# Kernel tuning notes

Hardware: AMD Instinct MI355X
Metric: run time of the kernel (lower is better)

Reference implementation:

```python
import jax, jax.numpy as jnp
import numpy as np

ROUTINGS = 3
EPS = 1e-7  # K.epsilon()


def squash(s, axis=-1):
    # v = (||s||^2 / (1 + ||s||^2)) * s / ||s||
    s_sq = jnp.sum(jnp.square(s), axis=axis, keepdims=True)
    scale = s_sq / (1.0 + s_sq) / jnp.sqrt(s_sq + EPS)
    return scale * s


def setup_inputs() -> dict:
    key = jax.random.key(0)
    k1, k2 = jax.random.split(key)
    B, num_in_caps, in_caps_dim = 32, 2048, 16
    num_caps, caps_dim = 64, 32
    input_tensor = jax.random.normal(k1, (B, num_in_caps, in_caps_dim), dtype=jnp.float32)
    # he_normal init: std = sqrt(2 / fan_in), fan_in = in_caps_dim (last axis contracted)
    fan_in = num_in_caps * caps_dim * in_caps_dim  # keras computes fan_in from receptive field; use simple he scale
    W = jax.random.normal(k2, (num_caps, num_in_caps, caps_dim, in_caps_dim), dtype=jnp.float32) * np.float32(np.sqrt(2.0 / in_caps_dim))
    return {"input_tensor": input_tensor, "W": W}


def reference(input_tensor, W):
    B = input_tensor.shape[0]
    num_caps, num_in_caps = W.shape[0], W.shape[1]
    # inputs_hat[b,j,i,c] = sum_d W[j,i,c,d] * x[b,i,d]  (fused einsum replacing map_fn+batch_dot)
    inputs_hat = jnp.einsum('bid,jicd->bjic', input_tensor, W)
    b = jnp.zeros((B, num_caps, num_in_caps), dtype=inputs_hat.dtype)
    # NOTE: source never updates b inside the loop, so every iteration is identical.
    activations = None
    for _ in range(ROUTINGS):
        c = jax.nn.softmax(b, axis=1)  # over num_caps axis, as tf.nn.softmax(b, dim=1)
        s = jnp.einsum('bji,bjic->bjc', c, inputs_hat)  # batch_dot(c, inputs_hat, [2,2])
        activations = squash(s)
    return activations
```

## Files before the change

kernel.cpp:

```cpp
#include <hip/hip_runtime.h>

typedef __attribute__((ext_vector_type(8)))  short bf16x8;
typedef __attribute__((ext_vector_type(16))) float f32x16;
typedef __attribute__((ext_vector_type(4)))  int   i32x4;

__device__ __forceinline__ unsigned cvt2(float lo, float hi) {
    unsigned r;
    asm volatile("v_cvt_pk_bf16_f32 %0, %1, %2" : "=v"(r) : "v"(lo), "v"(hi));
    return r;
}
__device__ __forceinline__ bf16x8 pack8(float4 a, float4 b) {
    union { i32x4 i; bf16x8 h; } c;
    c.i.x = cvt2(a.x, a.y);
    c.i.y = cvt2(a.z, a.w);
    c.i.z = cvt2(b.x, b.y);
    c.i.w = cvt2(b.z, b.w);
    return c.h;
}

__global__ void caps_init(float* __restrict__ ws) {
    ws[blockIdx.x * 256 + threadIdx.x] = 0.0f;
}

template<int MODE>
__global__ __launch_bounds__(256, 4)
void caps_mfma(const float* __restrict__ x, const float* __restrict__ W,
               float* __restrict__ ws)
{
    const int tid  = threadIdx.x;
    const int w    = tid >> 6;
    const int lane = tid & 63;
    const int m    = lane & 31;
    const int h    = lane >> 5;

    const int j     = blockIdx.x >> 4;
    const int ic    = blockIdx.x & 15;
    const int ibase = ic * 128;

    const char* Wb = (const char*)W + (((size_t)(j * 2048 + ibase + w)) << 11)
                   + (m << 6) + (h << 5);
    const char* Xb = (const char*)x + ((size_t)m << 17) + ((ibase + w) << 6) + (h << 5);

    f32x16 acc = {};

    float4 wv[4][2], xv[4][2];
#pragma unroll
    for (int s = 0; s < 4; ++s) {
        wv[s][0] = *(const float4*)(Wb + s * 8192);
        wv[s][1] = *(const float4*)(Wb + s * 8192 + 16);
        xv[s][0] = *(const float4*)(Xb + s * 256);
        xv[s][1] = *(const float4*)(Xb + s * 256 + 16);
    }

#pragma unroll 1
    for (int t = 0; t < 28; t += 4) {
#pragma unroll
        for (int s = 0; s < 4; ++s) {
            bf16x8 afrag = pack8(xv[s][0], xv[s][1]);
            bf16x8 bfrag = pack8(wv[s][0], wv[s][1]);
            wv[s][0] = *(const float4*)(Wb + (s + 4) * 8192);
            wv[s][1] = *(const float4*)(Wb + (s + 4) * 8192 + 16);
            xv[s][0] = *(const float4*)(Xb + (s + 4) * 256);
            xv[s][1] = *(const float4*)(Xb + (s + 4) * 256 + 16);
            acc = __builtin_amdgcn_mfma_f32_32x32x16_bf16(afrag, bfrag, acc, 0, 0, 0);
        }
        Wb += 4 * 8192; Xb += 4 * 256;
    }
#pragma unroll
    for (int s = 0; s < 4; ++s)
        acc = __builtin_amdgcn_mfma_f32_32x32x16_bf16(
                  pack8(xv[s][0], xv[s][1]), pack8(wv[s][0], wv[s][1]), acc, 0, 0, 0);

    __shared__ float red[4096];
#pragma unroll
    for (int r = 0; r < 16; ++r)
        red[w * 1024 + r * 64 + lane] = acc[r];
    __syncthreads();

#pragma unroll
    for (int e = 0; e < 4; ++e) {
        int idx = e * 256 + tid;
        int b = idx >> 5, c = idx & 31;
        int l = (((b >> 2) & 1) << 5) + c;
        int r = (b & 3) | (((b >> 3) & 3) << 2);
        float s = red[r * 64 + l] + red[1024 + r * 64 + l]
                + red[2048 + r * 64 + l] + red[3072 + r * 64 + l];
        if (MODE == 0)
            ws[(ic * 32 + b) * 2048 + j * 32 + c] = s;
        else
            atomicAdd(&ws[b * 2048 + j * 32 + c], s);
    }
}

template<int NIC>
__global__ void caps_finalize(const float* __restrict__ ws, float* __restrict__ out) {
    int o = blockIdx.x * 256 + threadIdx.x;
    int b = o >> 11;
    int rest = o & 2047;
    float v = 0.0f;
#pragma unroll
    for (int k = 0; k < NIC; ++k) v += ws[(k * 32 + b) * 2048 + rest];
    v *= (1.0f / 64.0f);
    float sq = v * v;
    sq += __shfl_xor(sq, 1, 64);
    sq += __shfl_xor(sq, 2, 64);
    sq += __shfl_xor(sq, 4, 64);
    sq += __shfl_xor(sq, 8, 64);
    sq += __shfl_xor(sq, 16, 64);
    float scale = sq / (1.0f + sq) / sqrtf(sq + 1e-7f);
    out[o] = scale * v;
}

__global__ void caps_finalize_a(const float* __restrict__ ws, float* __restrict__ out) {
    int o = blockIdx.x * 256 + threadIdx.x;
    float v = ws[o] * (1.0f / 64.0f);
    float sq = v * v;
    sq += __shfl_xor(sq, 1, 64);
    sq += __shfl_xor(sq, 2, 64);
    sq += __shfl_xor(sq, 4, 64);
    sq += __shfl_xor(sq, 8, 64);
    sq += __shfl_xor(sq, 16, 64);
    float scale = sq / (1.0f + sq) / sqrtf(sq + 1e-7f);
    out[o] = scale * v;
}

extern "C" void kernel_launch(void* const* d_in, const int* in_sizes, int n_in,
                              void* d_out, int out_size, void* d_ws, size_t ws_size,
                              hipStream_t stream) {
    (void)in_sizes; (void)n_in; (void)out_size;
    const float* x = (const float*)d_in[0];
    const float* W = (const float*)d_in[1];
    float* out = (float*)d_out;
    float* ws  = (float*)d_ws;

    if (ws_size >= (size_t)16 * 65536 * sizeof(float)) {
        hipLaunchKernelGGL((caps_mfma<0>),     dim3(1024), dim3(256), 0, stream, x, W, ws);
        hipLaunchKernelGGL((caps_finalize<16>),dim3(256),  dim3(256), 0, stream, ws, out);
    } else {
        float* acc_buf = (ws_size >= (size_t)65536 * sizeof(float)) ? ws : out;
        hipLaunchKernelGGL(caps_init,          dim3(256),  dim3(256), 0, stream, acc_buf);
        hipLaunchKernelGGL((caps_mfma<1>),     dim3(1024), dim3(256), 0, stream, x, W, acc_buf);
        hipLaunchKernelGGL(caps_finalize_a,    dim3(256),  dim3(256), 0, stream, acc_buf, out);
    }
}
```

Before: 60.70 us.

## Pre-convert x to bf16 fragment layout and halve input-capsule chunk size

Adds a pre-pass kernel that converts x to bf16 and stores it in the exact per-lane MFMA A-fragment order. The main kernel then loads x with one contiguous 16-byte load per step instead of strided fp32 gathers plus conversion. The i-chunk size also drops from 128 to 64, doubling the grid to 2048 blocks for more parallelism. The cost is an extra launch, a larger workspace slab, and twice the partial sums for finalize to reduce.

```diff
diff --git a/kernel.cpp b/kernel.cpp
--- a/kernel.cpp
+++ b/kernel.cpp
@@ -18,58 +18,87 @@
     return c.h;
 }
 
+__global__ void caps_xconv(const float* __restrict__ x, uint4* __restrict__ xf) {
+    int g = blockIdx.x * 256 + threadIdx.x;
+    int i = g >> 6, l = g & 63;
+    int b = l & 31, h = l >> 5;
+    const float4* p = (const float4*)(x + (b * 2048 + i) * 16 + h * 8);
+    float4 a = p[0], q = p[1];
+    uint4 o;
+    o.x = cvt2(a.x, a.y); o.y = cvt2(a.z, a.w);
+    o.z = cvt2(q.x, q.y); o.w = cvt2(q.z, q.w);
+    xf[g] = o;
+}
+
 __global__ void caps_init(float* __restrict__ ws) {
     ws[blockIdx.x * 256 + threadIdx.x] = 0.0f;
 }
 
-template<int MODE>
+template<int MODE, int GATHER, int ICHUNK>
 __global__ __launch_bounds__(256, 4)
 void caps_mfma(const float* __restrict__ x, const float* __restrict__ W,
-               float* __restrict__ ws)
+               float* __restrict__ ws, const char* __restrict__ xf)
 {
+    constexpr int NIC = 2048 / ICHUNK;
+    constexpr int NT  = ICHUNK / 4;
+
     const int tid  = threadIdx.x;
     const int w    = tid >> 6;
     const int lane = tid & 63;
     const int m    = lane & 31;
     const int h    = lane >> 5;
 
-    const int j     = blockIdx.x >> 4;
-    const int ic    = blockIdx.x & 15;
-    const int ibase = ic * 128;
+    const int j     = blockIdx.x / NIC;
+    const int ic    = blockIdx.x % NIC;
+    const int ibase = ic * ICHUNK;
 
     const char* Wb = (const char*)W + (((size_t)(j * 2048 + ibase + w)) << 11)
                    + (m << 6) + (h << 5);
     const char* Xb = (const char*)x + ((size_t)m << 17) + ((ibase + w) << 6) + (h << 5);
+    const char* Xf = xf + ((ibase + w) << 10) + (lane << 4);
 
     f32x16 acc = {};
 
-    float4 wv[4][2], xv[4][2];
+    float4 wv[4][2];
+    bf16x8 xa[4];
+    float4 xg[4][2];
+
 #pragma unroll
     for (int s = 0; s < 4; ++s) {
         wv[s][0] = *(const float4*)(Wb + s * 8192);
         wv[s][1] = *(const float4*)(Wb + s * 8192 + 16);
-        xv[s][0] = *(const float4*)(Xb + s * 256);
-        xv[s][1] = *(const float4*)(Xb + s * 256 + 16);
+        if (GATHER) {
+            xg[s][0] = *(const float4*)(Xb + s * 256);
+            xg[s][1] = *(const float4*)(Xb + s * 256 + 16);
+        } else {
+            xa[s] = *(const bf16x8*)(Xf + s * 4096);
+        }
     }
 
 #pragma unroll 1
-    for (int t = 0; t < 28; t += 4) {
+    for (int t = 0; t < NT - 4; t += 4) {
 #pragma unroll
         for (int s = 0; s < 4; ++s) {
-            bf16x8 afrag = pack8(xv[s][0], xv[s][1]);
+            bf16x8 afrag = GATHER ? pack8(xg[s][0], xg[s][1]) : xa[s];
             bf16x8 bfrag = pack8(wv[s][0], wv[s][1]);
             wv[s][0] = *(const float4*)(Wb + (s + 4) * 8192);
             wv[s][1] = *(const float4*)(Wb + (s + 4) * 8192 + 16);
-            xv[s][0] = *(const float4*)(Xb + (s + 4) * 256);
-            xv[s][1] = *(const float4*)(Xb + (s + 4) * 256 + 16);
+            if (GATHER) {
+                xg[s][0] = *(const float4*)(Xb + (s + 4) * 256);
+                xg[s][1] = *(const float4*)(Xb + (s + 4) * 256 + 16);
+            } else {
+                xa[s] = *(const bf16x8*)(Xf + (s + 4) * 4096);
+            }
             acc = __builtin_amdgcn_mfma_f32_32x32x16_bf16(afrag, bfrag, acc, 0, 0, 0);
         }
-        Wb += 4 * 8192; Xb += 4 * 256;
+        Wb += 4 * 8192; Xb += 4 * 256; Xf += 4 * 4096;
     }
 #pragma unroll
-    for (int s = 0; s < 4; ++s)
+    for (int s = 0; s < 4; ++s) {
+        bf16x8 afrag = GATHER ? pack8(xg[s][0], xg[s][1]) : xa[s];
         acc = __builtin_amdgcn_mfma_f32_32x32x16_bf16(
-                  pack8(xv[s][0], xv[s][1]), pack8(wv[s][0], wv[s][1]), acc, 0, 0, 0);
+                  afrag, pack8(wv[s][0], wv[s][1]), acc, 0, 0, 0);
+    }
 
     __shared__ float red[4096];
 #pragma unroll
@@ -133,13 +162,21 @@
     float* out = (float*)d_out;
     float* ws  = (float*)d_ws;
 
-    if (ws_size >= (size_t)16 * 65536 * sizeof(float)) {
-        hipLaunchKernelGGL((caps_mfma<0>),     dim3(1024), dim3(256), 0, stream, x, W, ws);
-        hipLaunchKernelGGL((caps_finalize<16>),dim3(256),  dim3(256), 0, stream, ws, out);
+    const size_t slab_f = (size_t)32 * 32 * 2048;
+    const size_t need   = slab_f * 4 + (size_t)2048 * 1024;
+
+    if (ws_size >= need) {
+        char* xf = (char*)(ws + slab_f);
+        hipLaunchKernelGGL(caps_xconv,            dim3(512),  dim3(256), 0, stream, x, (uint4*)xf);
+        hipLaunchKernelGGL((caps_mfma<0, 0, 64>), dim3(2048), dim3(256), 0, stream, x, W, ws, xf);
+        hipLaunchKernelGGL((caps_finalize<32>),   dim3(256),  dim3(256), 0, stream, ws, out);
+    } else if (ws_size >= (size_t)16 * 65536 * sizeof(float)) {
+        hipLaunchKernelGGL((caps_mfma<0, 1, 128>), dim3(1024), dim3(256), 0, stream, x, W, ws, (const char*)0);
+        hipLaunchKernelGGL((caps_finalize<16>),    dim3(256),  dim3(256), 0, stream, ws, out);
     } else {
         float* acc_buf = (ws_size >= (size_t)65536 * sizeof(float)) ? ws : out;
-        hipLaunchKernelGGL(caps_init,          dim3(256),  dim3(256), 0, stream, acc_buf);
-        hipLaunchKernelGGL((caps_mfma<1>),     dim3(1024), dim3(256), 0, stream, x, W, acc_buf);
-        hipLaunchKernelGGL(caps_finalize_a,    dim3(256),  dim3(256), 0, stream, acc_buf, out);
+        hipLaunchKernelGGL(caps_init,              dim3(256),  dim3(256), 0, stream, acc_buf);
+        hipLaunchKernelGGL((caps_mfma<1, 1, 128>), dim3(1024), dim3(256), 0, stream, x, W, acc_buf, (const char*)0);
+        hipLaunchKernelGGL(caps_finalize_a,        dim3(256),  dim3(256), 0, stream, acc_buf, out);
     }
 }
```

New measurement: 52.87 us. 12.9% less time.
